# Kernel tuning notes

Measured on AMD Instinct MI355X. Metric: run time of the kernel, lower is better.

## Reference

```python
import math
import jax, jax.numpy as jnp
import numpy as np

B, T, D = 4, 4096, 1024


def setup_inputs() -> dict:
    key = jax.random.key(0)
    k_x, k_wr, k_br, k_wi, k_bi = jax.random.split(key, 5)
    s = 1.0 / math.sqrt(D)  # torch Linear default init range
    x = jax.random.normal(k_x, (B, T, D), dtype=jnp.float32)
    h0 = jnp.zeros((B, D), dtype=jnp.float32)
    W_r = jax.random.uniform(k_wr, (D, D), jnp.float32, -s, s)
    b_r = jax.random.uniform(k_br, (D,), jnp.float32, -s, s)
    W_i = jax.random.uniform(k_wi, (D, D), jnp.float32, -s, s)
    b_i = jax.random.uniform(k_bi, (D,), jnp.float32, -s, s)
    Lambda = jnp.linspace(math.log(0.01), math.log(0.99), D).astype(jnp.float32)
    return {"x": x, "h0": h0, "W_r": W_r, "b_r": b_r, "W_i": W_i, "b_i": b_i, "Lambda": Lambda}


def reference(x, h0, W_r, b_r, W_i, b_i, Lambda):
    # Gates are pointwise in t -> compute them for the whole sequence at once.
    # torch Linear: y = x @ W.T + b
    r = jax.nn.sigmoid(jnp.einsum('btd,ed->bte', x, W_r) + b_r)   # (B,T,D)
    i = jax.nn.sigmoid(jnp.einsum('btd,ed->bte', x, W_i) + b_i)   # (B,T,D)
    decay = 8.0 * jax.nn.softplus(Lambda)                          # (D,)
    a = jnp.exp(-decay * r)                                        # (B,T,D)
    scale = jnp.sqrt(jnp.clip(1.0 - a * a, 0.0, None))             # (B,T,D)
    gx = scale * (i * x)                                           # gated input

    def step(h, ins):
        a_t, gx_t = ins          # each (B,D)
        h = a_t * h + gx_t
        return h, h

    a_tb = jnp.swapaxes(a, 0, 1)    # (T,B,D)
    gx_tb = jnp.swapaxes(gx, 0, 1)  # (T,B,D)
    h_T, ys = jax.lax.scan(step, h0, (a_tb, gx_tb))
    output_seq = jnp.swapaxes(ys, 0, 1)  # (B,T,D)
    return output_seq, h_T
```

## Files before the change

### kernel.cpp

```cpp
#include <hip/hip_runtime.h>


#define B_ 4
#define T_ 4096
#define D_ 1024
#define BT_ (B_ * T_)
#define NC_ 64
#define L_ (T_ / NC_)

#define BMR 256
#define BNC 128
#define BKT 64
#define NT_ (D_ / BKT)
#define BUFB 65536

typedef float v4f __attribute__((ext_vector_type(4)));
typedef __bf16 v8bf __attribute__((ext_vector_type(8)));
typedef unsigned int u32;

__device__ inline unsigned short f2bf(float f) {
    unsigned int u = __float_as_uint(f);
    u += 0x7FFFu + ((u >> 16) & 1u);
    return (unsigned short)(u >> 16);
}

__device__ inline ushort4 f2bf4(float4 v) {
    return make_ushort4(f2bf(v.x), f2bf(v.y), f2bf(v.z), f2bf(v.w));
}

__device__ inline void gload16(const void* g, void* l) {
    __builtin_amdgcn_global_load_lds(
        (const __attribute__((address_space(1))) u32*)g,
        (__attribute__((address_space(3))) u32*)l, 16, 0, 0);
}

__global__ void prep_kernel(const float4* __restrict__ x4,
                            const float4* __restrict__ wr4,
                            const float4* __restrict__ wi4,
                            const float* __restrict__ lam,
                            ushort4* __restrict__ xb4,
                            ushort4* __restrict__ wrb4,
                            ushort4* __restrict__ wib4,
                            float* __restrict__ decay) {
    const int n = gridDim.x * blockDim.x;
    const int tid = blockIdx.x * blockDim.x + threadIdx.x;
    const int nx4 = (BT_ * D_) / 4;
    const int nw4 = (D_ * D_) / 4;
    for (int i = tid; i < nx4; i += n) xb4[i] = f2bf4(x4[i]);
    for (int i = tid; i < nw4; i += n) {
        wrb4[i] = f2bf4(wr4[i]);
        wib4[i] = f2bf4(wi4[i]);
    }
    for (int i = tid; i < D_; i += n) {
        float sp = log1pf(expf(lam[i]));
        decay[i] = 8.0f * sp;
    }
}

__global__ __launch_bounds__(512, 2) void gemm_gates(
    const unsigned short* __restrict__ xb,
    const unsigned short* __restrict__ wrb,
    const unsigned short* __restrict__ wib,
    const float* __restrict__ br,
    const float* __restrict__ bi,
    const float* __restrict__ decay,
    const float* __restrict__ x,
    float* __restrict__ a_buf,
    float* __restrict__ gx_out) {
    __shared__ __align__(16) char lds[2 * BUFB];

    const int tid = threadIdx.x;
    const int lane = tid & 63;
    const int wave = tid >> 6;
    const int wr = wave >> 2;
    const int wc = wave & 3;
    const int lr = lane & 15;
    const int lg = lane >> 4;
    const int rowbase = blockIdx.x * BMR;
    const int colbase = blockIdx.y * BNC;

    const int srow = tid >> 3;
    const int kslot = (tid & 7) ^ (srow & 7);

    const unsigned short* gAq[4];
#pragma unroll
    for (int q = 0; q < 4; ++q)
        gAq[q] = xb + (size_t)(rowbase + q * 64 + srow) * D_ + kslot * 8;
    const unsigned short* gBq[4];
    gBq[0] = wrb + (size_t)(colbase + srow) * D_ + kslot * 8;
    gBq[1] = wib + (size_t)(colbase + srow) * D_ + kslot * 8;
    gBq[2] = wrb + (size_t)(colbase + 64 + srow) * D_ + kslot * 8;
    gBq[3] = wib + (size_t)(colbase + 64 + srow) * D_ + kslot * 8;

#define STG_A(nb, q, kel) gload16(gAq[q] + (kel), lds + (nb) * BUFB + (q) * 8192 + wave * 1024)
#define STG_B(nb, q, kel) gload16(gBq[q] + (kel), lds + (nb) * BUFB + 32768 + (q) * 8192 + wave * 1024)

    const int bo = (wc & 1) * 32;
    const int bstrip = wc >> 1;

    v4f ar[8][2], ai[8][2];
#pragma unroll
    for (int mi = 0; mi < 8; ++mi)
#pragma unroll
        for (int nf = 0; nf < 2; ++nf)
#pragma unroll
            for (int j = 0; j < 4; ++j) { ar[mi][nf][j] = 0.0f; ai[mi][nf][j] = 0.0f; }

    v8bf cbr[2], cbi[2];

    STG_A(0, 0, 0); STG_A(0, 1, 0); STG_A(0, 2, 0); STG_A(0, 3, 0);
    STG_B(0, 0, 0); STG_B(0, 1, 0); STG_B(0, 2, 0); STG_B(0, 3, 0);
    __builtin_amdgcn_sched_barrier(0);
    asm volatile("s_waitcnt vmcnt(0)");
    __builtin_amdgcn_s_barrier();

#define PHASE(lb, KS, MH, PRECODE)                                              \
    do {                                                                        \
        if ((MH) == 0) {                                                        \
            _Pragma("unroll")                                                   \
            for (int nf = 0; nf < 2; ++nf) {                                    \
                const int brr = bstrip * 128 + bo + nf * 16 + lr;               \
                cbr[nf] = *(const v8bf*)((lb) + 32768 + brr * 128 +             \
                                         (((KS) * 4 + lg) ^ (brr & 7)) * 16);   \
                const int bri = brr + 64;                                       \
                cbi[nf] = *(const v8bf*)((lb) + 32768 + bri * 128 +             \
                                         (((KS) * 4 + lg) ^ (bri & 7)) * 16);   \
            }                                                                   \
        }                                                                       \
        v8bf af[4];                                                             \
        _Pragma("unroll")                                                       \
        for (int m4 = 0; m4 < 4; ++m4) {                                        \
            const int row = wr * 128 + ((MH) * 4 + m4) * 16 + lr;               \
            af[m4] = *(const v8bf*)((lb) + row * 128 +                          \
                                    (((KS) * 4 + lg) ^ (row & 7)) * 16);        \
        }                                                                       \
        PRECODE;                                                                \
        __builtin_amdgcn_sched_barrier(0);                                      \
        __builtin_amdgcn_s_barrier();                                           \
        __builtin_amdgcn_s_setprio(1);                                          \
        _Pragma("unroll")                                                       \
        for (int m4 = 0; m4 < 4; ++m4)                                          \
            _Pragma("unroll")                                                   \
            for (int nf = 0; nf < 2; ++nf) {                                    \
                ar[(MH) * 4 + m4][nf] = __builtin_amdgcn_mfma_f32_16x16x32_bf16( \
                    af[m4], cbr[nf], ar[(MH) * 4 + m4][nf], 0, 0, 0);           \
                ai[(MH) * 4 + m4][nf] = __builtin_amdgcn_mfma_f32_16x16x32_bf16( \
                    af[m4], cbi[nf], ai[(MH) * 4 + m4][nf], 0, 0, 0);           \
            }                                                                   \
        __builtin_amdgcn_s_setprio(0);                                          \
        __builtin_amdgcn_sched_barrier(0);                                      \
        __builtin_amdgcn_s_barrier();                                           \
    } while (0)

    for (int t = 0; t < NT_; ++t) {
        const int sw = t & 1;
        const int nb = sw ^ 1;
        const char* lb = lds + sw * BUFB;
        const int knext = (t + 1) * BKT;
        const bool more = (t + 1 < NT_);

        PHASE(lb, 0, 0,
              if (more) {
                  STG_B(nb, 0, knext); STG_B(nb, 1, knext);
                  __builtin_amdgcn_sched_barrier(0);
                  asm volatile("s_waitcnt vmcnt(2)");
              } else {
                  __builtin_amdgcn_sched_barrier(0);
                  asm volatile("s_waitcnt vmcnt(0)");
              });
        PHASE(lb, 0, 1,
              if (more) { STG_B(nb, 2, knext); STG_B(nb, 3, knext); });
        PHASE(lb, 1, 0,
              if (more) { STG_A(nb, 0, knext); STG_A(nb, 2, knext); });
        PHASE(lb, 1, 1,
              if (more) {
                  STG_A(nb, 1, knext); STG_A(nb, 3, knext);
                  __builtin_amdgcn_sched_barrier(0);
                  asm volatile("s_waitcnt vmcnt(2)");
              });
    }
#undef PHASE
#undef STG_A
#undef STG_B

#pragma unroll
    for (int nf = 0; nf < 2; ++nf) {
        const int gcol = colbase + wc * 32 + nf * 16 + lr;
        const float brv = br[gcol];
        const float biv = bi[gcol];
        const float dec = decay[gcol];
#pragma unroll
        for (int mi = 0; mi < 8; ++mi) {
#pragma unroll
            for (int rr = 0; rr < 4; ++rr) {
                const int grow = rowbase + wr * 128 + mi * 16 + lg * 4 + rr;
                const size_t o = (size_t)grow * D_ + gcol;
                const float zr = ar[mi][nf][rr] + brv;
                const float zi = ai[mi][nf][rr] + biv;
                const float rg = 1.0f / (1.0f + __expf(-zr));
                const float ig = 1.0f / (1.0f + __expf(-zi));
                const float av = __expf(-dec * rg);
                const float sc = sqrtf(fmaxf(1.0f - av * av, 0.0f));
                const float xv = x[o];
                a_buf[o] = av;
                gx_out[o] = sc * (ig * xv);
            }
        }
    }
}

__global__ __launch_bounds__(256) void scan1(const float* __restrict__ a,
                                             const float* __restrict__ gx,
                                             float* __restrict__ P,
                                             float* __restrict__ H) {
    const int idx = blockIdx.x * 256 + threadIdx.x;
    const int d = idx & (D_ - 1);
    const int c = (idx >> 10) & (NC_ - 1);
    const int b = idx >> 16;
    const size_t base = ((size_t)b * T_ + c * L_) * D_ + d;
    float p = 1.0f, h = 0.0f;
    for (int t = 0; t < L_; ++t) {
        const float at = a[base + (size_t)t * D_];
        const float g = gx[base + (size_t)t * D_];
        p *= at;
        h = at * h + g;
    }
    P[idx] = p;
    H[idx] = h;
}

__global__ __launch_bounds__(256) void combine(const float* __restrict__ P,
                                               const float* __restrict__ H,
                                               const float* __restrict__ h0,
                                               float* __restrict__ hstart,
                                               float* __restrict__ hT) {
    const int idx = blockIdx.x * 256 + threadIdx.x;
    const int d = idx & (D_ - 1);
    const int b = idx >> 10;
    float h = h0[b * D_ + d];
    for (int c = 0; c < NC_; ++c) {
        const int o = (b * NC_ + c) * D_ + d;
        hstart[o] = h;
        h = P[o] * h + H[o];
    }
    hT[b * D_ + d] = h;
}

__global__ __launch_bounds__(256) void scan2(const float* __restrict__ a,
                                             float* __restrict__ out,
                                             const float* __restrict__ hstart) {
    const int idx = blockIdx.x * 256 + threadIdx.x;
    const int d = idx & (D_ - 1);
    const int c = (idx >> 10) & (NC_ - 1);
    const int b = idx >> 16;
    const size_t base = ((size_t)b * T_ + c * L_) * D_ + d;
    float h = hstart[idx];
    for (int t = 0; t < L_; ++t) {
        const size_t o = base + (size_t)t * D_;
        h = a[o] * h + out[o];
        out[o] = h;
    }
}

extern "C" void kernel_launch(void* const* d_in, const int* in_sizes, int n_in,
                              void* d_out, int out_size, void* d_ws, size_t ws_size,
                              hipStream_t stream) {
    const float* x   = (const float*)d_in[0];
    const float* h0  = (const float*)d_in[1];
    const float* Wr  = (const float*)d_in[2];
    const float* br  = (const float*)d_in[3];
    const float* Wi  = (const float*)d_in[4];
    const float* bi  = (const float*)d_in[5];
    const float* lam = (const float*)d_in[6];
    float* out = (float*)d_out;

    char* ws = (char*)d_ws;
    unsigned short* xb  = (unsigned short*)ws; ws += (size_t)BT_ * D_ * 2;
    unsigned short* wrb = (unsigned short*)ws; ws += (size_t)D_ * D_ * 2;
    unsigned short* wib = (unsigned short*)ws; ws += (size_t)D_ * D_ * 2;
    float* decay  = (float*)ws;  ws += (size_t)D_ * 4;
    float* a_buf  = (float*)ws;  ws += (size_t)BT_ * D_ * 4;
    float* P      = (float*)ws;  ws += (size_t)B_ * NC_ * D_ * 4;
    float* Hc     = (float*)ws;  ws += (size_t)B_ * NC_ * D_ * 4;
    float* hstart = (float*)ws;

    prep_kernel<<<2048, 256, 0, stream>>>(
        (const float4*)x, (const float4*)Wr, (const float4*)Wi, lam,
        (ushort4*)xb, (ushort4*)wrb, (ushort4*)wib, decay);

    gemm_gates<<<dim3(BT_ / BMR, D_ / BNC), 512, 0, stream>>>(
        xb, wrb, wib, br, bi, decay, x, a_buf, out);

    scan1<<<(B_ * NC_ * D_) / 256, 256, 0, stream>>>(a_buf, out, P, Hc);

    combine<<<(B_ * D_) / 256, 256, 0, stream>>>(P, Hc, h0, hstart, out + (size_t)BT_ * D_);

    scan2<<<(B_ * NC_ * D_) / 256, 256, 0, stream>>>(a_buf, out, hstart);
}
```

Measured before the change: 166.7 us.

## Fuse chunk scan into GEMM epilogue and pack a/gx as fp16 pairs

Result: faster. 137.6 us (-17.4%).

```diff
diff --git a/kernel.cpp b/kernel.cpp
--- a/kernel.cpp
+++ b/kernel.cpp
@@ -13,6 +13,7 @@
 #define BKT 64
 #define NT_ (D_ / BKT)
 #define BUFB 65536
+#define STASH_STRIDE 132
 
 typedef float v4f __attribute__((ext_vector_type(4)));
 typedef __bf16 v8bf __attribute__((ext_vector_type(8)));
@@ -26,6 +27,25 @@
 
 __device__ inline ushort4 f2bf4(float4 v) {
     return make_ushort4(f2bf(v.x), f2bf(v.y), f2bf(v.z), f2bf(v.w));
+}
+
+__device__ inline u32 pack_ag(float a, float g) {
+    _Float16 ah = (_Float16)a, gh = (_Float16)g;
+    unsigned short au, gu;
+    __builtin_memcpy(&au, &ah, 2);
+    __builtin_memcpy(&gu, &gh, 2);
+    return ((u32)gu << 16) | au;
+}
+__device__ inline float unpack_a(u32 v) {
+    unsigned short u = (unsigned short)(v & 0xffffu);
+    _Float16 h; __builtin_memcpy(&h, &u, 2); return (float)h;
+}
+__device__ inline float unpack_g(u32 v) {
+    unsigned short u = (unsigned short)(v >> 16);
+    _Float16 h; __builtin_memcpy(&h, &u, 2); return (float)h;
+}
+__device__ inline float bf2f(unsigned short u) {
+    return __uint_as_float((u32)u << 16);
 }
 
 __device__ inline void gload16(const void* g, void* l) {
@@ -64,10 +84,10 @@
     const float* __restrict__ br,
     const float* __restrict__ bi,
     const float* __restrict__ decay,
-    const float* __restrict__ x,
-    float* __restrict__ a_buf,
-    float* __restrict__ gx_out) {
-    __shared__ __align__(16) char lds[2 * BUFB];
+    u32* __restrict__ ag,
+    float* __restrict__ P,
+    float* __restrict__ H) {
+    __shared__ __align__(16) char lds[256 * STASH_STRIDE * 4];
 
     const int tid = threadIdx.x;
     const int lane = tid & 63;
@@ -193,7 +213,8 @@
         for (int mi = 0; mi < 8; ++mi) {
 #pragma unroll
             for (int rr = 0; rr < 4; ++rr) {
-                const int grow = rowbase + wr * 128 + mi * 16 + lg * 4 + rr;
+                const int rl = wr * 128 + mi * 16 + lg * 4 + rr;
+                const int grow = rowbase + rl;
                 const size_t o = (size_t)grow * D_ + gcol;
                 const float zr = ar[mi][nf][rr] + brv;
                 const float zi = ai[mi][nf][rr] + biv;
@@ -201,32 +222,34 @@
                 const float ig = 1.0f / (1.0f + __expf(-zi));
                 const float av = __expf(-dec * rg);
                 const float sc = sqrtf(fmaxf(1.0f - av * av, 0.0f));
-                const float xv = x[o];
-                a_buf[o] = av;
-                gx_out[o] = sc * (ig * xv);
+                const float xv = bf2f(xb[o]);
+                const float gv = sc * (ig * xv);
+                const u32 pk = pack_ag(av, gv);
+                ag[o] = pk;
+                const int cl = wc * 32 + nf * 16 + lr;
+                *(u32*)(lds + (size_t)(rl * STASH_STRIDE + cl) * 4) = pk;
             }
         }
     }
-}
-
-__global__ __launch_bounds__(256) void scan1(const float* __restrict__ a,
-                                             const float* __restrict__ gx,
-                                             float* __restrict__ P,
-                                             float* __restrict__ H) {
-    const int idx = blockIdx.x * 256 + threadIdx.x;
-    const int d = idx & (D_ - 1);
-    const int c = (idx >> 10) & (NC_ - 1);
-    const int b = idx >> 16;
-    const size_t base = ((size_t)b * T_ + c * L_) * D_ + d;
-    float p = 1.0f, h = 0.0f;
-    for (int t = 0; t < L_; ++t) {
-        const float at = a[base + (size_t)t * D_];
-        const float g = gx[base + (size_t)t * D_];
-        p *= at;
-        h = at * h + g;
-    }
-    P[idx] = p;
-    H[idx] = h;
+    __syncthreads();
+
+    {
+        const int c = tid >> 7;
+        const int j = tid & 127;
+        const char* sb = lds + (size_t)(c * 64 * STASH_STRIDE + j) * 4;
+        float p = 1.0f, h = 0.0f;
+#pragma unroll 8
+        for (int t = 0; t < 64; ++t) {
+            const u32 v = *(const u32*)(sb + (size_t)t * STASH_STRIDE * 4);
+            const float a_ = unpack_a(v);
+            const float g_ = unpack_g(v);
+            p *= a_;
+            h = a_ * h + g_;
+        }
+        const int gc = (rowbase >> 6) + c;
+        P[(size_t)gc * D_ + colbase + j] = p;
+        H[(size_t)gc * D_ + colbase + j] = h;
+    }
 }
 
 __global__ __launch_bounds__(256) void combine(const float* __restrict__ P,
@@ -246,7 +269,7 @@
     hT[b * D_ + d] = h;
 }
 
-__global__ __launch_bounds__(256) void scan2(const float* __restrict__ a,
+__global__ __launch_bounds__(256) void scan2(const u32* __restrict__ ag,
                                              float* __restrict__ out,
                                              const float* __restrict__ hstart) {
     const int idx = blockIdx.x * 256 + threadIdx.x;
@@ -255,9 +278,11 @@
     const int b = idx >> 16;
     const size_t base = ((size_t)b * T_ + c * L_) * D_ + d;
     float h = hstart[idx];
+#pragma unroll 4
     for (int t = 0; t < L_; ++t) {
         const size_t o = base + (size_t)t * D_;
-        h = a[o] * h + out[o];
+        const u32 v = ag[o];
+        h = unpack_a(v) * h + unpack_g(v);
         out[o] = h;
     }
 }
@@ -279,7 +304,7 @@
     unsigned short* wrb = (unsigned short*)ws; ws += (size_t)D_ * D_ * 2;
     unsigned short* wib = (unsigned short*)ws; ws += (size_t)D_ * D_ * 2;
     float* decay  = (float*)ws;  ws += (size_t)D_ * 4;
-    float* a_buf  = (float*)ws;  ws += (size_t)BT_ * D_ * 4;
+    u32* ag       = (u32*)ws;    ws += (size_t)BT_ * D_ * 4;
     float* P      = (float*)ws;  ws += (size_t)B_ * NC_ * D_ * 4;
     float* Hc     = (float*)ws;  ws += (size_t)B_ * NC_ * D_ * 4;
     float* hstart = (float*)ws;
@@ -289,11 +314,9 @@
         (ushort4*)xb, (ushort4*)wrb, (ushort4*)wib, decay);
 
     gemm_gates<<<dim3(BT_ / BMR, D_ / BNC), 512, 0, stream>>>(
-        xb, wrb, wib, br, bi, decay, x, a_buf, out);
-
-    scan1<<<(B_ * NC_ * D_) / 256, 256, 0, stream>>>(a_buf, out, P, Hc);
+        xb, wrb, wib, br, bi, decay, ag, P, Hc);
 
     combine<<<(B_ * D_) / 256, 256, 0, stream>>>(P, Hc, h0, hstart, out + (size_t)BT_ * D_);
 
-    scan2<<<(B_ * NC_ * D_) / 256, 256, 0, stream>>>(a_buf, out, hstart);
-}
+    scan2<<<(B_ * NC_ * D_) / 256, 256, 0, stream>>>(ag, out, hstart);
+}
```

## Fuse gate GEMM and chunked scan into one cooperative kernel with grid syncs

Applied to the files above, without the earlier changes.

Measured after the change: 387.8 us. 2.33x slower.

```diff
diff --git a/kernel.cpp b/kernel.cpp
--- a/kernel.cpp
+++ b/kernel.cpp
@@ -1,4 +1,7 @@
 #include <hip/hip_runtime.h>
+#include <hip/hip_cooperative_groups.h>
+
+namespace cg = cooperative_groups;
 
 
 #define B_ 4
@@ -6,10 +9,8 @@
 #define D_ 1024
 #define BT_ (B_ * T_)
 #define NC_ 64
-#define L_ (T_ / NC_)
 
 #define BMR 256
-#define BNC 128
 #define BKT 64
 #define NT_ (D_ / BKT)
 #define BUFB 65536
@@ -23,11 +24,27 @@
     u += 0x7FFFu + ((u >> 16) & 1u);
     return (unsigned short)(u >> 16);
 }
-
 __device__ inline ushort4 f2bf4(float4 v) {
     return make_ushort4(f2bf(v.x), f2bf(v.y), f2bf(v.z), f2bf(v.w));
 }
-
+__device__ inline u32 pack2(float p, float h) {
+    _Float16 ph = (_Float16)p, hh = (_Float16)h;
+    unsigned short pu, hu;
+    __builtin_memcpy(&pu, &ph, 2);
+    __builtin_memcpy(&hu, &hh, 2);
+    return ((u32)hu << 16) | pu;
+}
+__device__ inline float unp_lo(u32 v) {
+    unsigned short u = (unsigned short)(v & 0xffffu);
+    _Float16 h; __builtin_memcpy(&h, &u, 2); return (float)h;
+}
+__device__ inline float unp_hi(u32 v) {
+    unsigned short u = (unsigned short)(v >> 16);
+    _Float16 h; __builtin_memcpy(&h, &u, 2); return (float)h;
+}
+__device__ inline float bf2f(unsigned short u) {
+    return __uint_as_float((u32)u << 16);
+}
 __device__ inline void gload16(const void* g, void* l) {
     __builtin_amdgcn_global_load_lds(
         (const __attribute__((address_space(1))) u32*)g,
@@ -57,16 +74,18 @@
     }
 }
 
-__global__ __launch_bounds__(512, 2) void gemm_gates(
+__global__ __launch_bounds__(512, 2) void fused(
     const unsigned short* __restrict__ xb,
     const unsigned short* __restrict__ wrb,
     const unsigned short* __restrict__ wib,
     const float* __restrict__ br,
     const float* __restrict__ bi,
     const float* __restrict__ decay,
-    const float* __restrict__ x,
-    float* __restrict__ a_buf,
-    float* __restrict__ gx_out) {
+    const float* __restrict__ h0,
+    float* __restrict__ Pg,
+    float* __restrict__ Hg,
+    float* __restrict__ hstart,
+    float* __restrict__ out) {
     __shared__ __align__(16) char lds[2 * BUFB];
 
     const int tid = threadIdx.x;
@@ -76,8 +95,9 @@
     const int wc = wave & 3;
     const int lr = lane & 15;
     const int lg = lane >> 4;
-    const int rowbase = blockIdx.x * BMR;
-    const int colbase = blockIdx.y * BNC;
+    const int bid = blockIdx.x;
+    const int colpair = bid & 3;
+    const int rowbase = (bid >> 2) * BMR;
 
     const int srow = tid >> 3;
     const int kslot = (tid & 7) ^ (srow & 7);
@@ -86,33 +106,38 @@
 #pragma unroll
     for (int q = 0; q < 4; ++q)
         gAq[q] = xb + (size_t)(rowbase + q * 64 + srow) * D_ + kslot * 8;
-    const unsigned short* gBq[4];
-    gBq[0] = wrb + (size_t)(colbase + srow) * D_ + kslot * 8;
-    gBq[1] = wib + (size_t)(colbase + srow) * D_ + kslot * 8;
-    gBq[2] = wrb + (size_t)(colbase + 64 + srow) * D_ + kslot * 8;
-    gBq[3] = wib + (size_t)(colbase + 64 + srow) * D_ + kslot * 8;
+    const unsigned short* gB0[4];
+    const unsigned short* gB1[4];
+    {
+        const int c0 = colpair * 256;
+        gB0[0] = wrb + (size_t)(c0 + srow) * D_ + kslot * 8;
+        gB0[1] = wib + (size_t)(c0 + srow) * D_ + kslot * 8;
+        gB0[2] = wrb + (size_t)(c0 + 64 + srow) * D_ + kslot * 8;
+        gB0[3] = wib + (size_t)(c0 + 64 + srow) * D_ + kslot * 8;
+        gB1[0] = gB0[0] + (size_t)128 * D_;
+        gB1[1] = gB0[1] + (size_t)128 * D_;
+        gB1[2] = gB0[2] + (size_t)128 * D_;
+        gB1[3] = gB0[3] + (size_t)128 * D_;
+    }
 
 #define STG_A(nb, q, kel) gload16(gAq[q] + (kel), lds + (nb) * BUFB + (q) * 8192 + wave * 1024)
-#define STG_B(nb, q, kel) gload16(gBq[q] + (kel), lds + (nb) * BUFB + 32768 + (q) * 8192 + wave * 1024)
+#define STG_B(nb, q, kel, GB) gload16(GB[q] + (kel), lds + (nb) * BUFB + 32768 + (q) * 8192 + wave * 1024)
 
     const int bo = (wc & 1) * 32;
     const int bstrip = wc >> 1;
 
     v4f ar[8][2], ai[8][2];
-#pragma unroll
-    for (int mi = 0; mi < 8; ++mi)
-#pragma unroll
-        for (int nf = 0; nf < 2; ++nf)
-#pragma unroll
-            for (int j = 0; j < 4; ++j) { ar[mi][nf][j] = 0.0f; ai[mi][nf][j] = 0.0f; }
-
     v8bf cbr[2], cbi[2];
-
-    STG_A(0, 0, 0); STG_A(0, 1, 0); STG_A(0, 2, 0); STG_A(0, 3, 0);
-    STG_B(0, 0, 0); STG_B(0, 1, 0); STG_B(0, 2, 0); STG_B(0, 3, 0);
-    __builtin_amdgcn_sched_barrier(0);
-    asm volatile("s_waitcnt vmcnt(0)");
-    __builtin_amdgcn_s_barrier();
+    u32 pk0[2][2][4][4];
+    u32 pk1[2][2][4][4];
+
+#define ZERO_ACC()                                                           \
+    do {                                                                     \
+        _Pragma("unroll") for (int mi = 0; mi < 8; ++mi)                     \
+            _Pragma("unroll") for (int nf = 0; nf < 2; ++nf)                 \
+                _Pragma("unroll") for (int j = 0; j < 4; ++j) {              \
+                    ar[mi][nf][j] = 0.0f; ai[mi][nf][j] = 0.0f; }            \
+    } while (0)
 
 #define PHASE(lb, KS, MH, PRECODE)                                              \
     do {                                                                        \
@@ -152,114 +177,181 @@
         __builtin_amdgcn_s_barrier();                                           \
     } while (0)
 
-    for (int t = 0; t < NT_; ++t) {
-        const int sw = t & 1;
-        const int nb = sw ^ 1;
-        const char* lb = lds + sw * BUFB;
-        const int knext = (t + 1) * BKT;
-        const bool more = (t + 1 < NT_);
-
-        PHASE(lb, 0, 0,
-              if (more) {
-                  STG_B(nb, 0, knext); STG_B(nb, 1, knext);
-                  __builtin_amdgcn_sched_barrier(0);
-                  asm volatile("s_waitcnt vmcnt(2)");
-              } else {
-                  __builtin_amdgcn_sched_barrier(0);
-                  asm volatile("s_waitcnt vmcnt(0)");
-              });
-        PHASE(lb, 0, 1,
-              if (more) { STG_B(nb, 2, knext); STG_B(nb, 3, knext); });
-        PHASE(lb, 1, 0,
-              if (more) { STG_A(nb, 0, knext); STG_A(nb, 2, knext); });
-        PHASE(lb, 1, 1,
-              if (more) {
-                  STG_A(nb, 1, knext); STG_A(nb, 3, knext);
-                  __builtin_amdgcn_sched_barrier(0);
-                  asm volatile("s_waitcnt vmcnt(2)");
-              });
-    }
+#define KLOOP(GB)                                                               \
+    for (int t = 0; t < NT_; ++t) {                                             \
+        const int sw = t & 1;                                                   \
+        const int nb = sw ^ 1;                                                  \
+        const char* lb = lds + sw * BUFB;                                       \
+        const int knext = (t + 1) * BKT;                                        \
+        const bool more = (t + 1 < NT_);                                        \
+        PHASE(lb, 0, 0,                                                         \
+              if (more) {                                                       \
+                  STG_B(nb, 0, knext, GB); STG_B(nb, 1, knext, GB);             \
+                  __builtin_amdgcn_sched_barrier(0);                            \
+                  asm volatile("s_waitcnt vmcnt(2)");                           \
+              } else {                                                          \
+                  __builtin_amdgcn_sched_barrier(0);                            \
+                  asm volatile("s_waitcnt vmcnt(0)");                           \
+              });                                                               \
+        PHASE(lb, 0, 1,                                                         \
+              if (more) { STG_B(nb, 2, knext, GB); STG_B(nb, 3, knext, GB); }); \
+        PHASE(lb, 1, 0,                                                         \
+              if (more) { STG_A(nb, 0, knext); STG_A(nb, 2, knext); });         \
+        PHASE(lb, 1, 1,                                                         \
+              if (more) {                                                       \
+                  STG_A(nb, 1, knext); STG_A(nb, 3, knext);                     \
+                  __builtin_amdgcn_sched_barrier(0);                            \
+                  asm volatile("s_waitcnt vmcnt(2)");                           \
+              });                                                               \
+    }
+
+#define EPILOGUE(P, PK)                                                         \
+    do {                                                                        \
+        _Pragma("unroll")                                                       \
+        for (int nf = 0; nf < 2; ++nf) {                                        \
+            const int gcol = colpair * 256 + (P) * 128 + wc * 32 + nf * 16 + lr;\
+            const float brv = br[gcol];                                         \
+            const float biv = bi[gcol];                                         \
+            const float dec = decay[gcol];                                      \
+            _Pragma("unroll")                                                   \
+            for (int half = 0; half < 2; ++half) {                              \
+                float Sp = 1.0f, Sh = 0.0f;                                     \
+                _Pragma("unroll")                                               \
+                for (int m4 = 0; m4 < 4; ++m4) {                                \
+                    const int mi = half * 4 + m4;                               \
+                    float av[4], gv[4];                                         \
+                    _Pragma("unroll")                                           \
+                    for (int rr = 0; rr < 4; ++rr) {                            \
+                        const int grow = rowbase + wr * 128 + mi * 16 + lg * 4 + rr; \
+                        const float zr = ar[mi][nf][rr] + brv;                  \
+                        const float zi = ai[mi][nf][rr] + biv;                  \
+                        const float rg = 1.0f / (1.0f + __expf(-zr));           \
+                        const float ig = 1.0f / (1.0f + __expf(-zi));           \
+                        av[rr] = __expf(-dec * rg);                             \
+                        const float sc = sqrtf(fmaxf(1.0f - av[rr] * av[rr], 0.0f)); \
+                        const float xv = bf2f(xb[(size_t)grow * D_ + gcol]);    \
+                        gv[rr] = sc * (ig * xv);                                \
+                    }                                                           \
+                                            \
+                    float lp = (av[0] * av[1]) * (av[2] * av[3]);               \
+                    float lh = gv[0];                                           \
+                    lh = av[1] * lh + gv[1];                                    \
+                    lh = av[2] * lh + gv[2];                                    \
+                    lh = av[3] * lh + gv[3];                                    \
+                            \
+                    float cp = lp, ch = lh;                                     \
+                    {                                                           \
+                        const float pp = __shfl_up(cp, 16, 64);                 \
+                        const float ph = __shfl_up(ch, 16, 64);                 \
+                        if (lg >= 1) { ch = cp * ph + ch; cp = pp * cp; }       \
+                    }                                                           \
+                    {                                                           \
+                        const float pp = __shfl_up(cp, 32, 64);                 \
+                        const float ph = __shfl_up(ch, 32, 64);                 \
+                        if (lg >= 2) { ch = cp * ph + ch; cp = pp * cp; }       \
+                    }                                                           \
+                                                       \
+                    float ep = __shfl_up(cp, 16, 64);                           \
+                    float eh = __shfl_up(ch, 16, 64);                           \
+                    if (lg == 0) { ep = 1.0f; eh = 0.0f; }                      \
+                                  \
+                    float wp = Sp * ep;                                         \
+                    float wh = ep * Sh + eh;                                    \
+                    _Pragma("unroll")                                           \
+                    for (int rr = 0; rr < 4; ++rr) {                            \
+                        wh = av[rr] * wh + gv[rr];                              \
+                        wp = wp * av[rr];                                       \
+                        PK[nf][half][m4][rr] = pack2(wp, wh);                   \
+                    }                                                           \
+                            \
+                    const float fp3 = __shfl(cp, 48 + lr, 64);                  \
+                    const float fh3 = __shfl(ch, 48 + lr, 64);                  \
+                    Sh = fp3 * Sh + fh3;                                        \
+                    Sp = Sp * fp3;                                              \
+                }                                                               \
+                if (lg == 0) {                                                  \
+                    const int gc = (rowbase >> 6) + wr * 2 + half;              \
+                    Pg[(size_t)gc * D_ + gcol] = Sp;                            \
+                    Hg[(size_t)gc * D_ + gcol] = Sh;                            \
+                }                                                               \
+            }                                                                   \
+        }                                                                       \
+    } while (0)
+
+    ZERO_ACC();
+    STG_A(0, 0, 0); STG_A(0, 1, 0); STG_A(0, 2, 0); STG_A(0, 3, 0);
+    STG_B(0, 0, 0, gB0); STG_B(0, 1, 0, gB0); STG_B(0, 2, 0, gB0); STG_B(0, 3, 0, gB0);
+    __builtin_amdgcn_sched_barrier(0);
+    asm volatile("s_waitcnt vmcnt(0)");
+    __builtin_amdgcn_s_barrier();
+    KLOOP(gB0);
+
+    STG_A(0, 0, 0); STG_A(0, 1, 0); STG_A(0, 2, 0); STG_A(0, 3, 0);
+    STG_B(0, 0, 0, gB1); STG_B(0, 1, 0, gB1); STG_B(0, 2, 0, gB1); STG_B(0, 3, 0, gB1);
+
+    EPILOGUE(0, pk0);
+
+    __builtin_amdgcn_sched_barrier(0);
+    asm volatile("s_waitcnt vmcnt(0)");
+    __builtin_amdgcn_s_barrier();
+
+    ZERO_ACC();
+    KLOOP(gB1);
+    EPILOGUE(1, pk1);
+
+    cg::grid_group grid = cg::this_grid();
+    __threadfence();
+    grid.sync();
+
+    if (bid < 8) {
+        const int idx = bid * 512 + tid;
+        const int d = idx & (D_ - 1);
+        const int b = idx >> 10;
+        float h = h0[b * D_ + d];
+        for (int c = 0; c < NC_; ++c) {
+            const size_t o = (size_t)(b * NC_ + c) * D_ + d;
+            hstart[o] = h;
+            h = Pg[o] * h + Hg[o];
+        }
+        out[(size_t)BT_ * D_ + b * D_ + d] = h;
+    }
+    __threadfence();
+    grid.sync();
+
+#define RESCAN(P, PK)                                                           \
+    do {                                                                        \
+        _Pragma("unroll")                                                       \
+        for (int nf = 0; nf < 2; ++nf) {                                        \
+            const int gcol = colpair * 256 + (P) * 128 + wc * 32 + nf * 16 + lr;\
+            _Pragma("unroll")                                                   \
+            for (int half = 0; half < 2; ++half) {                              \
+                const int gc = (rowbase >> 6) + wr * 2 + half;                  \
+                const float hc = hstart[(size_t)gc * D_ + gcol];                \
+                _Pragma("unroll")                                               \
+                for (int m4 = 0; m4 < 4; ++m4) {                                \
+                    _Pragma("unroll")                                           \
+                    for (int rr = 0; rr < 4; ++rr) {                            \
+                        const int grow = rowbase + wr * 128 +                   \
+                                         (half * 4 + m4) * 16 + lg * 4 + rr;    \
+                        const u32 v = PK[nf][half][m4][rr];                     \
+                        out[(size_t)grow * D_ + gcol] =                         \
+                            unp_hi(v) + unp_lo(v) * hc;                         \
+                    }                                                           \
+                }                                                               \
+            }                                                                   \
+        }                                                                       \
+    } while (0)
+
+    RESCAN(0, pk0);
+    RESCAN(1, pk1);
+
+#undef RESCAN
+#undef EPILOGUE
+#undef KLOOP
 #undef PHASE
+#undef ZERO_ACC
 #undef STG_A
 #undef STG_B
-
-#pragma unroll
-    for (int nf = 0; nf < 2; ++nf) {
-        const int gcol = colbase + wc * 32 + nf * 16 + lr;
-        const float brv = br[gcol];
-        const float biv = bi[gcol];
-        const float dec = decay[gcol];
-#pragma unroll
-        for (int mi = 0; mi < 8; ++mi) {
-#pragma unroll
-            for (int rr = 0; rr < 4; ++rr) {
-                const int grow = rowbase + wr * 128 + mi * 16 + lg * 4 + rr;
-                const size_t o = (size_t)grow * D_ + gcol;
-                const float zr = ar[mi][nf][rr] + brv;
-                const float zi = ai[mi][nf][rr] + biv;
-                const float rg = 1.0f / (1.0f + __expf(-zr));
-                const float ig = 1.0f / (1.0f + __expf(-zi));
-                const float av = __expf(-dec * rg);
-                const float sc = sqrtf(fmaxf(1.0f - av * av, 0.0f));
-                const float xv = x[o];
-                a_buf[o] = av;
-                gx_out[o] = sc * (ig * xv);
-            }
-        }
-    }
-}
-
-__global__ __launch_bounds__(256) void scan1(const float* __restrict__ a,
-                                             const float* __restrict__ gx,
-                                             float* __restrict__ P,
-                                             float* __restrict__ H) {
-    const int idx = blockIdx.x * 256 + threadIdx.x;
-    const int d = idx & (D_ - 1);
-    const int c = (idx >> 10) & (NC_ - 1);
-    const int b = idx >> 16;
-    const size_t base = ((size_t)b * T_ + c * L_) * D_ + d;
-    float p = 1.0f, h = 0.0f;
-    for (int t = 0; t < L_; ++t) {
-        const float at = a[base + (size_t)t * D_];
-        const float g = gx[base + (size_t)t * D_];
-        p *= at;
-        h = at * h + g;
-    }
-    P[idx] = p;
-    H[idx] = h;
-}
-
-__global__ __launch_bounds__(256) void combine(const float* __restrict__ P,
-                                               const float* __restrict__ H,
-                                               const float* __restrict__ h0,
-                                               float* __restrict__ hstart,
-                                               float* __restrict__ hT) {
-    const int idx = blockIdx.x * 256 + threadIdx.x;
-    const int d = idx & (D_ - 1);
-    const int b = idx >> 10;
-    float h = h0[b * D_ + d];
-    for (int c = 0; c < NC_; ++c) {
-        const int o = (b * NC_ + c) * D_ + d;
-        hstart[o] = h;
-        h = P[o] * h + H[o];
-    }
-    hT[b * D_ + d] = h;
-}
-
-__global__ __launch_bounds__(256) void scan2(const float* __restrict__ a,
-                                             float* __restrict__ out,
-                                             const float* __restrict__ hstart) {
-    const int idx = blockIdx.x * 256 + threadIdx.x;
-    const int d = idx & (D_ - 1);
-    const int c = (idx >> 10) & (NC_ - 1);
-    const int b = idx >> 16;
-    const size_t base = ((size_t)b * T_ + c * L_) * D_ + d;
-    float h = hstart[idx];
-    for (int t = 0; t < L_; ++t) {
-        const size_t o = base + (size_t)t * D_;
-        h = a[o] * h + out[o];
-        out[o] = h;
-    }
 }
 
 extern "C" void kernel_launch(void* const* d_in, const int* in_sizes, int n_in,
@@ -279,21 +371,28 @@
     unsigned short* wrb = (unsigned short*)ws; ws += (size_t)D_ * D_ * 2;
     unsigned short* wib = (unsigned short*)ws; ws += (size_t)D_ * D_ * 2;
     float* decay  = (float*)ws;  ws += (size_t)D_ * 4;
-    float* a_buf  = (float*)ws;  ws += (size_t)BT_ * D_ * 4;
-    float* P      = (float*)ws;  ws += (size_t)B_ * NC_ * D_ * 4;
-    float* Hc     = (float*)ws;  ws += (size_t)B_ * NC_ * D_ * 4;
+    float* Pg     = (float*)ws;  ws += (size_t)B_ * NC_ * D_ * 4;
+    float* Hg     = (float*)ws;  ws += (size_t)B_ * NC_ * D_ * 4;
     float* hstart = (float*)ws;
 
     prep_kernel<<<2048, 256, 0, stream>>>(
         (const float4*)x, (const float4*)Wr, (const float4*)Wi, lam,
         (ushort4*)xb, (ushort4*)wrb, (ushort4*)wib, decay);
 
-    gemm_gates<<<dim3(BT_ / BMR, D_ / BNC), 512, 0, stream>>>(
-        xb, wrb, wib, br, bi, decay, x, a_buf, out);
-
-    scan1<<<(B_ * NC_ * D_) / 256, 256, 0, stream>>>(a_buf, out, P, Hc);
-
-    combine<<<(B_ * D_) / 256, 256, 0, stream>>>(P, Hc, h0, hstart, out + (size_t)BT_ * D_);
-
-    scan2<<<(B_ * NC_ * D_) / 256, 256, 0, stream>>>(a_buf, out, hstart);
-}
+    {
+        const unsigned short* a0 = xb;
+        const unsigned short* a1 = wrb;
+        const unsigned short* a2 = wib;
+        const float* a3 = br;
+        const float* a4 = bi;
+        const float* a5 = decay;
+        const float* a6 = h0;
+        float* a7 = Pg;
+        float* a8 = Hg;
+        float* a9 = hstart;
+        float* a10 = out;
+        void* args[] = {&a0, &a1, &a2, &a3, &a4, &a5, &a6, &a7, &a8, &a9, &a10};
+        hipLaunchCooperativeKernel((const void*)fused, dim3(256), dim3(512),
+                                   args, 0, stream);
+    }
+}
```

## Fuse chunk-local scan into GEMM epilogue and store packed fp16 prefix states

Applied to the files above, without the earlier changes.

New measurement: 143.6 us. -13.8%, faster.

```diff
diff --git a/kernel.cpp b/kernel.cpp
--- a/kernel.cpp
+++ b/kernel.cpp
@@ -6,7 +6,6 @@
 #define D_ 1024
 #define BT_ (B_ * T_)
 #define NC_ 64
-#define L_ (T_ / NC_)
 
 #define BMR 256
 #define BNC 128
@@ -23,11 +22,27 @@
     u += 0x7FFFu + ((u >> 16) & 1u);
     return (unsigned short)(u >> 16);
 }
-
 __device__ inline ushort4 f2bf4(float4 v) {
     return make_ushort4(f2bf(v.x), f2bf(v.y), f2bf(v.z), f2bf(v.w));
 }
-
+__device__ inline u32 pack2(float p, float h) {
+    _Float16 ph = (_Float16)p, hh = (_Float16)h;
+    unsigned short pu, hu;
+    __builtin_memcpy(&pu, &ph, 2);
+    __builtin_memcpy(&hu, &hh, 2);
+    return ((u32)hu << 16) | pu;
+}
+__device__ inline float unp_lo(u32 v) {
+    unsigned short u = (unsigned short)(v & 0xffffu);
+    _Float16 h; __builtin_memcpy(&h, &u, 2); return (float)h;
+}
+__device__ inline float unp_hi(u32 v) {
+    unsigned short u = (unsigned short)(v >> 16);
+    _Float16 h; __builtin_memcpy(&h, &u, 2); return (float)h;
+}
+__device__ inline float bf2f(unsigned short u) {
+    return __uint_as_float((u32)u << 16);
+}
 __device__ inline void gload16(const void* g, void* l) {
     __builtin_amdgcn_global_load_lds(
         (const __attribute__((address_space(1))) u32*)g,
@@ -64,9 +79,9 @@
     const float* __restrict__ br,
     const float* __restrict__ bi,
     const float* __restrict__ decay,
-    const float* __restrict__ x,
-    float* __restrict__ a_buf,
-    float* __restrict__ gx_out) {
+    u32* __restrict__ ag,
+    float* __restrict__ Pg,
+    float* __restrict__ Hg) {
     __shared__ __align__(16) char lds[2 * BUFB];
 
     const int tid = threadIdx.x;
@@ -162,22 +177,15 @@
         PHASE(lb, 0, 0,
               if (more) {
                   STG_B(nb, 0, knext); STG_B(nb, 1, knext);
-                  __builtin_amdgcn_sched_barrier(0);
-                  asm volatile("s_waitcnt vmcnt(2)");
-              } else {
-                  __builtin_amdgcn_sched_barrier(0);
-                  asm volatile("s_waitcnt vmcnt(0)");
+                  STG_B(nb, 2, knext); STG_B(nb, 3, knext);
+                  STG_A(nb, 0, knext); STG_A(nb, 1, knext);
+                  STG_A(nb, 2, knext); STG_A(nb, 3, knext);
               });
-        PHASE(lb, 0, 1,
-              if (more) { STG_B(nb, 2, knext); STG_B(nb, 3, knext); });
-        PHASE(lb, 1, 0,
-              if (more) { STG_A(nb, 0, knext); STG_A(nb, 2, knext); });
+        PHASE(lb, 0, 1, );
+        PHASE(lb, 1, 0, );
         PHASE(lb, 1, 1,
-              if (more) {
-                  STG_A(nb, 1, knext); STG_A(nb, 3, knext);
-                  __builtin_amdgcn_sched_barrier(0);
-                  asm volatile("s_waitcnt vmcnt(2)");
-              });
+              __builtin_amdgcn_sched_barrier(0);
+              asm volatile("s_waitcnt vmcnt(0)"););
     }
 #undef PHASE
 #undef STG_A
@@ -190,43 +198,63 @@
         const float biv = bi[gcol];
         const float dec = decay[gcol];
 #pragma unroll
-        for (int mi = 0; mi < 8; ++mi) {
-#pragma unroll
-            for (int rr = 0; rr < 4; ++rr) {
-                const int grow = rowbase + wr * 128 + mi * 16 + lg * 4 + rr;
-                const size_t o = (size_t)grow * D_ + gcol;
-                const float zr = ar[mi][nf][rr] + brv;
-                const float zi = ai[mi][nf][rr] + biv;
-                const float rg = 1.0f / (1.0f + __expf(-zr));
-                const float ig = 1.0f / (1.0f + __expf(-zi));
-                const float av = __expf(-dec * rg);
-                const float sc = sqrtf(fmaxf(1.0f - av * av, 0.0f));
-                const float xv = x[o];
-                a_buf[o] = av;
-                gx_out[o] = sc * (ig * xv);
+        for (int half = 0; half < 2; ++half) {
+            float Sp = 1.0f, Sh = 0.0f;
+#pragma unroll
+            for (int m4 = 0; m4 < 4; ++m4) {
+                const int mi = half * 4 + m4;
+                float av[4], gv[4];
+#pragma unroll
+                for (int rr = 0; rr < 4; ++rr) {
+                    const int grow = rowbase + wr * 128 + mi * 16 + lg * 4 + rr;
+                    const float zr = ar[mi][nf][rr] + brv;
+                    const float zi = ai[mi][nf][rr] + biv;
+                    const float rg = 1.0f / (1.0f + __expf(-zr));
+                    const float ig = 1.0f / (1.0f + __expf(-zi));
+                    av[rr] = __expf(-dec * rg);
+                    const float sc = sqrtf(fmaxf(1.0f - av[rr] * av[rr], 0.0f));
+                    gv[rr] = sc * (ig * bf2f(xb[(size_t)grow * D_ + gcol]));
+                }
+                float lp = (av[0] * av[1]) * (av[2] * av[3]);
+                float lh = gv[0];
+                lh = av[1] * lh + gv[1];
+                lh = av[2] * lh + gv[2];
+                lh = av[3] * lh + gv[3];
+                float cp = lp, ch = lh;
+                {
+                    const float pp = __shfl_up(cp, 16, 64);
+                    const float ph = __shfl_up(ch, 16, 64);
+                    if (lg >= 1) { ch = cp * ph + ch; cp = pp * cp; }
+                }
+                {
+                    const float pp = __shfl_up(cp, 32, 64);
+                    const float ph = __shfl_up(ch, 32, 64);
+                    if (lg >= 2) { ch = cp * ph + ch; cp = pp * cp; }
+                }
+                float ep = __shfl_up(cp, 16, 64);
+                float eh = __shfl_up(ch, 16, 64);
+                if (lg == 0) { ep = 1.0f; eh = 0.0f; }
+                float wp = Sp * ep;
+                float wh = ep * Sh + eh;
+#pragma unroll
+                for (int rr = 0; rr < 4; ++rr) {
+                    wh = av[rr] * wh + gv[rr];
+                    wp = wp * av[rr];
+                    const int grow = rowbase + wr * 128 + mi * 16 + lg * 4 + rr;
+                    ag[(size_t)grow * D_ + gcol] = pack2(wp, wh);
+                }
+                const float fp3 = __shfl(cp, 48 + lr, 64);
+                const float fh3 = __shfl(ch, 48 + lr, 64);
+                Sh = fp3 * Sh + fh3;
+                Sp = Sp * fp3;
+            }
+            if (lg == 0) {
+                const int gc = (rowbase >> 6) + wr * 2 + half;
+                Pg[(size_t)gc * D_ + gcol] = Sp;
+                Hg[(size_t)gc * D_ + gcol] = Sh;
             }
         }
     }
-}
-
-__global__ __launch_bounds__(256) void scan1(const float* __restrict__ a,
-                                             const float* __restrict__ gx,
-                                             float* __restrict__ P,
-                                             float* __restrict__ H) {
-    const int idx = blockIdx.x * 256 + threadIdx.x;
-    const int d = idx & (D_ - 1);
-    const int c = (idx >> 10) & (NC_ - 1);
-    const int b = idx >> 16;
-    const size_t base = ((size_t)b * T_ + c * L_) * D_ + d;
-    float p = 1.0f, h = 0.0f;
-    for (int t = 0; t < L_; ++t) {
-        const float at = a[base + (size_t)t * D_];
-        const float g = gx[base + (size_t)t * D_];
-        p *= at;
-        h = at * h + g;
-    }
-    P[idx] = p;
-    H[idx] = h;
 }
 
 __global__ __launch_bounds__(256) void combine(const float* __restrict__ P,
@@ -246,19 +274,24 @@
     hT[b * D_ + d] = h;
 }
 
-__global__ __launch_bounds__(256) void scan2(const float* __restrict__ a,
-                                             float* __restrict__ out,
-                                             const float* __restrict__ hstart) {
-    const int idx = blockIdx.x * 256 + threadIdx.x;
-    const int d = idx & (D_ - 1);
-    const int c = (idx >> 10) & (NC_ - 1);
-    const int b = idx >> 16;
-    const size_t base = ((size_t)b * T_ + c * L_) * D_ + d;
-    float h = hstart[idx];
-    for (int t = 0; t < L_; ++t) {
-        const size_t o = base + (size_t)t * D_;
-        h = a[o] * h + out[o];
-        out[o] = h;
+__global__ __launch_bounds__(256) void scan2(const uint4* __restrict__ ag4,
+                                             const float4* __restrict__ hs4,
+                                             float4* __restrict__ out4) {
+    const int n = (BT_ * D_) / 4;
+    const int stride = gridDim.x * 256;
+    for (int i = blockIdx.x * 256 + threadIdx.x; i < n; i += stride) {
+        const int d4 = i & (D_ / 4 - 1);
+        const int row = i >> 8;
+        const int b = row >> 12;
+        const int c = (row & (T_ - 1)) >> 6;
+        const float4 hs = hs4[(size_t)(b * NC_ + c) * (D_ / 4) + d4];
+        const uint4 v = ag4[i];
+        float4 o;
+        o.x = unp_hi(v.x) + unp_lo(v.x) * hs.x;
+        o.y = unp_hi(v.y) + unp_lo(v.y) * hs.y;
+        o.z = unp_hi(v.z) + unp_lo(v.z) * hs.z;
+        o.w = unp_hi(v.w) + unp_lo(v.w) * hs.w;
+        out4[i] = o;
     }
 }
 
@@ -279,9 +312,9 @@
     unsigned short* wrb = (unsigned short*)ws; ws += (size_t)D_ * D_ * 2;
     unsigned short* wib = (unsigned short*)ws; ws += (size_t)D_ * D_ * 2;
     float* decay  = (float*)ws;  ws += (size_t)D_ * 4;
-    float* a_buf  = (float*)ws;  ws += (size_t)BT_ * D_ * 4;
-    float* P      = (float*)ws;  ws += (size_t)B_ * NC_ * D_ * 4;
-    float* Hc     = (float*)ws;  ws += (size_t)B_ * NC_ * D_ * 4;
+    u32* ag       = (u32*)ws;    ws += (size_t)BT_ * D_ * 4;
+    float* Pg     = (float*)ws;  ws += (size_t)B_ * NC_ * D_ * 4;
+    float* Hg     = (float*)ws;  ws += (size_t)B_ * NC_ * D_ * 4;
     float* hstart = (float*)ws;
 
     prep_kernel<<<2048, 256, 0, stream>>>(
@@ -289,11 +322,9 @@
         (ushort4*)xb, (ushort4*)wrb, (ushort4*)wib, decay);
 
     gemm_gates<<<dim3(BT_ / BMR, D_ / BNC), 512, 0, stream>>>(
-        xb, wrb, wib, br, bi, decay, x, a_buf, out);
-
-    scan1<<<(B_ * NC_ * D_) / 256, 256, 0, stream>>>(a_buf, out, P, Hc);
-
-    combine<<<(B_ * D_) / 256, 256, 0, stream>>>(P, Hc, h0, hstart, out + (size_t)BT_ * D_);
-
-    scan2<<<(B_ * NC_ * D_) / 256, 256, 0, stream>>>(a_buf, out, hstart);
-}
+        xb, wrb, wib, br, bi, decay, ag, Pg, Hg);
+
+    combine<<<(B_ * D_) / 256, 256, 0, stream>>>(Pg, Hg, h0, hstart, out + (size_t)BT_ * D_);
+
+    scan2<<<2048, 256, 0, stream>>>((const uint4*)ag, (const float4*)hstart, (float4*)out);
+}
```
